# Optimization experiments

Hardware: AMD Instinct MI355X
Metric: run time of the kernel (lower is better)

## Reference

```python
import jax, jax.numpy as jnp
import numpy as np

B, L, C, H, FF = 4, 1024, 1024, 16, 4096
D = C // H  # head_dim = 64
SCALE = (D * 2.0) ** -0.5  # scale_factor = 2.0


def layer_norm(x, g, b, eps=1e-5):
    mu = jnp.mean(x, axis=-1, keepdims=True)
    var = jnp.var(x, axis=-1, keepdims=True)
    return (x - mu) * jax.lax.rsqrt(var + eps) * g + b


def setup_inputs() -> dict:
    key = jax.random.key(0)
    ks = jax.random.split(key, 12)
    s = 0.02
    inp = {
        'x': jax.random.normal(ks[0], (B, L, C), jnp.float32),
        'attn_bias': jax.random.normal(ks[1], (B, H, L, L), jnp.float32),
        'attention_mask': jnp.zeros((B, 1, L, L), jnp.float32),
        'Wq': jax.random.normal(ks[2], (C, C), jnp.float32) * s,
        'bq': jnp.zeros((C,), jnp.float32),
        'Wk': jax.random.normal(ks[3], (C, C), jnp.float32) * s,
        'bk': jnp.zeros((C,), jnp.float32),
        'Wv': jax.random.normal(ks[4], (C, C), jnp.float32) * s,
        'bv': jnp.zeros((C,), jnp.float32),
        'Wo': jax.random.normal(ks[5], (C, C), jnp.float32) * s,
        'bo': jnp.zeros((C,), jnp.float32),
        'c_attn': jnp.ones((H,), jnp.float32),
        'W1': jax.random.normal(ks[6], (FF, C), jnp.float32) * s,
        'b1': jnp.zeros((FF,), jnp.float32),
        'W2': jax.random.normal(ks[7], (C, FF), jnp.float32) * s,
        'b2': jnp.zeros((C,), jnp.float32),
        'attn_ln_g': jnp.ones((C,), jnp.float32),
        'attn_ln_b': jnp.zeros((C,), jnp.float32),
        'attn_mid_ln_g': jnp.ones((C,), jnp.float32),
        'attn_mid_ln_b': jnp.zeros((C,), jnp.float32),
        'ffn_ln_g': jnp.ones((C,), jnp.float32),
        'ffn_ln_b': jnp.zeros((C,), jnp.float32),
        'ffn_mid_ln_g': jnp.ones((FF,), jnp.float32),
        'ffn_mid_ln_b': jnp.zeros((FF,), jnp.float32),
    }
    return inp


def reference(x, attn_bias, attention_mask, Wq, bq, Wk, bk, Wv, bv, Wo, bo,
              c_attn, W1, b1, W2, b2, attn_ln_g, attn_ln_b,
              attn_mid_ln_g, attn_mid_ln_b, ffn_ln_g, ffn_ln_b,
              ffn_mid_ln_g, ffn_mid_ln_b):
    # ---- attention block (pre-norm, normformer) ----
    residual = x
    h = layer_norm(x, attn_ln_g, attn_ln_b)
    q = (h @ Wq.T + bq).reshape(B, L, H, D).transpose(0, 2, 1, 3)  # (B,H,L,D)
    k = (h @ Wk.T + bk).reshape(B, L, H, D).transpose(0, 2, 1, 3)
    v = (h @ Wv.T + bv).reshape(B, L, H, D).transpose(0, 2, 1, 3)
    # scores with bias (src_len == tgt_len, so the -src_len: slice is full) and mask
    scores = jnp.einsum('bhld,bhsd->bhls', q, k) * SCALE + attn_bias + attention_mask
    w = jax.nn.softmax(scores, axis=-1)
    attn = jnp.einsum('bhls,bhsd->bhld', w, v)
    attn = attn * c_attn[None, :, None, None]  # per-head scale (scale_heads)
    attn = attn.transpose(0, 2, 1, 3).reshape(B, L, C)
    attn = attn @ Wo.T + bo
    attn = layer_norm(attn, attn_mid_ln_g, attn_mid_ln_b)  # normformer mid-LN
    x = residual + attn
    # ---- FFN block (pre-norm, normformer) ----
    residual = x
    h = layer_norm(x, ffn_ln_g, ffn_ln_b)
    h = jax.nn.gelu(h @ W1.T + b1, approximate=False)
    h = layer_norm(h, ffn_mid_ln_g, ffn_mid_ln_b)  # normformer mid-LN on d_ff
    h = h @ W2.T + b2
    x = residual + h
    return x
```

## Files before the change

### kernel.cpp

```cpp
#include <hip/hip_runtime.h>
#include <hip/hip_bf16.h>
#include <math.h>

#define BB 4
#define LL 1024
#define CC 1024
#define HH 16
#define DD 64
#define FFD 4096
#define MM (BB*LL)
#define ATT_SCALE 0.08838834764831845f

typedef __bf16 bf16x8 __attribute__((ext_vector_type(8)));
typedef float f32x4 __attribute__((ext_vector_type(4)));

#define F32_PATTERN 0x3F800000u

__device__ __forceinline__ float b2f(unsigned short u) {
  union { unsigned int i; float f; } v; v.i = ((unsigned int)u) << 16; return v.f;
}
__device__ __forceinline__ unsigned short f2b(float f) {
  union { float f; unsigned int i; } v; v.f = f;
  unsigned int x = v.i;
  return (unsigned short)((x + 0x7fffu + ((x >> 16) & 1u)) >> 16);
}
__device__ __forceinline__ float ld1(const void* p, size_t i, bool isf32) {
  return isf32 ? reinterpret_cast<const float*>(p)[i]
               : b2f(reinterpret_cast<const unsigned short*>(p)[i]);
}
__device__ __forceinline__ float4 ld4(const void* p, size_t i, bool isf32) {
  float4 r;
  if (isf32) {
    r = *reinterpret_cast<const float4*>(reinterpret_cast<const float*>(p) + i);
  } else {
    ushort4 u = *reinterpret_cast<const ushort4*>(reinterpret_cast<const unsigned short*>(p) + i);
    r.x = b2f(u.x); r.y = b2f(u.y); r.z = b2f(u.z); r.w = b2f(u.w);
  }
  return r;
}
__device__ __forceinline__ float wave_sum(float v) {
#pragma unroll
  for (int o = 32; o > 0; o >>= 1) v += __shfl_down(v, o, 64);
  return v;
}

typedef __attribute__((address_space(1))) const void* as1cv;
typedef __attribute__((address_space(3))) void* as3v;
__device__ __forceinline__ void glds16(const void* g, void* l) {
  __builtin_amdgcn_global_load_lds((as1cv)g, (as3v)l, 16, 0, 0);
}

template <int COLS>
__global__ __launch_bounds__(256) void k_ln(
    const void* __restrict__ src, int srcext,
    const void* __restrict__ g, const void* __restrict__ bta,
    const void* __restrict__ res,
    unsigned short* __restrict__ dst,
    const unsigned int* __restrict__ probe)
{
  const bool isf32 = (*probe == F32_PATTERN);
  const bool sf = srcext && isf32;
  constexpr int NCH = COLS / 1024;
  const int row = blockIdx.x;
  const int t = threadIdx.x;
  const size_t base = (size_t)row * COLS;
  float fv[NCH * 4];
  float s = 0.f, s2 = 0.f;
#pragma unroll
  for (int c = 0; c < NCH; ++c) {
    float4 u = ld4(src, base + (size_t)(t + 256 * c) * 4, sf);
    fv[c * 4 + 0] = u.x; fv[c * 4 + 1] = u.y; fv[c * 4 + 2] = u.z; fv[c * 4 + 3] = u.w;
    s += u.x + u.y + u.z + u.w;
    s2 += u.x * u.x + u.y * u.y + u.z * u.z + u.w * u.w;
  }
  s = wave_sum(s); s2 = wave_sum(s2);
  __shared__ float red1[4], red2[4], stats[2];
  const int wv = t >> 6;
  if ((t & 63) == 0) { red1[wv] = s; red2[wv] = s2; }
  __syncthreads();
  if (t == 0) {
    float S = red1[0] + red1[1] + red1[2] + red1[3];
    float S2 = red2[0] + red2[1] + red2[2] + red2[3];
    float mu = S / COLS;
    float var = S2 / COLS - mu * mu;
    stats[0] = mu; stats[1] = rsqrtf(fmaxf(var, 0.f) + 1e-5f);
  }
  __syncthreads();
  const float mu = stats[0], rsg = stats[1];
#pragma unroll
  for (int c = 0; c < NCH; ++c) {
    const int off = (t + 256 * c) * 4;
    float4 gv = ld4(g, off, isf32);
    float4 bv = ld4(bta, off, isf32);
    float r0 = 0.f, r1 = 0.f, r2 = 0.f, r3 = 0.f;
    if (res) {
      float4 rv = ld4(res, base + off, isf32);
      r0 = rv.x; r1 = rv.y; r2 = rv.z; r3 = rv.w;
    }
    ushort4 o;
    o.x = f2b((fv[c * 4 + 0] - mu) * rsg * gv.x + bv.x + r0);
    o.y = f2b((fv[c * 4 + 1] - mu) * rsg * gv.y + bv.y + r1);
    o.z = f2b((fv[c * 4 + 2] - mu) * rsg * gv.z + bv.z + r2);
    o.w = f2b((fv[c * 4 + 3] - mu) * rsg * gv.w + bv.w + r3);
    *reinterpret_cast<ushort4*>(&dst[base + off]) = o;
  }
}

__global__ __launch_bounds__(256) void k_w2b(
    const void* __restrict__ Wq, const void* __restrict__ Wk,
    const void* __restrict__ Wv, const void* __restrict__ Wo,
    const void* __restrict__ W1, const void* __restrict__ W2,
    unsigned short* __restrict__ dst, const unsigned int* __restrict__ probe)
{
  const bool isf32 = (*probe == F32_PATTERN);
  const size_t NW = (size_t)CC * CC;
  const size_t i = ((size_t)blockIdx.x * 256 + threadIdx.x) * 8;
  const void* src; size_t off;
  if      (i <     NW) { src = Wq; off = i; }
  else if (i < 2 * NW) { src = Wk; off = i - NW; }
  else if (i < 3 * NW) { src = Wv; off = i - 2 * NW; }
  else if (i < 4 * NW) { src = Wo; off = i - 3 * NW; }
  else if (i < 8 * NW) { src = W1; off = i - 4 * NW; }
  else                 { src = W2; off = i - 8 * NW; }
  ushort4 lo, hi;
  if (isf32) {
    const float* f = reinterpret_cast<const float*>(src) + off;
    float4 u = *reinterpret_cast<const float4*>(f);
    float4 v = *reinterpret_cast<const float4*>(f + 4);
    lo.x = f2b(u.x); lo.y = f2b(u.y); lo.z = f2b(u.z); lo.w = f2b(u.w);
    hi.x = f2b(v.x); hi.y = f2b(v.y); hi.z = f2b(v.z); hi.w = f2b(v.w);
  } else {
    const unsigned short* u = reinterpret_cast<const unsigned short*>(src) + off;
    lo = *reinterpret_cast<const ushort4*>(u);
    hi = *reinterpret_cast<const ushort4*>(u + 4);
  }
  *reinterpret_cast<ushort4*>(&dst[i])     = lo;
  *reinterpret_cast<ushort4*>(&dst[i + 4]) = hi;
}

template <int EPI, int NT>
__device__ __forceinline__ void gemm_core(
    const unsigned short* __restrict__ A,
    const unsigned short* __restrict__ W,
    const void* __restrict__ bias,
    const unsigned short* __restrict__ res,
    void* __restrict__ out, int outext,
    int M, int N, int K, bool isf32)
{
  constexpr int BN = NT * 32;
  __shared__ __align__(16) unsigned short As[128][32];
  __shared__ __align__(16) unsigned short Bs[BN][32];
  const int t = threadIdx.x;
  const int wv = t >> 6, lane = t & 63;
  const int fr = lane & 15, kq = (lane >> 4) * 8;
  const int gx = gridDim.x;
  const int nwg = gx * gridDim.y;
  int lin = blockIdx.y * gx + blockIdx.x;
  if ((nwg & 7) == 0) lin = (lin & 7) * (nwg >> 3) + (lin >> 3);
  const int m0 = (lin / gx) * 128, n0 = (lin % gx) * BN;
  const int wr = (wv >> 1) * 64, wc = (wv & 1) * (BN / 2);

  f32x4 acc[4][NT];
#pragma unroll
  for (int i = 0; i < 4; ++i)
#pragma unroll
    for (int j = 0; j < NT; ++j) acc[i][j] = (f32x4){0.f, 0.f, 0.f, 0.f};

  const int sr = t >> 2, sc = (t & 3) * 8;
  const unsigned short* ga = &A[(size_t)(m0 + sr) * K + sc];
  const unsigned short* gb = &W[(size_t)(n0 + sr) * K + sc];
  unsigned short* la = &As[0][0] + t * 8;
  unsigned short* lb = &Bs[0][0] + t * 8;
  const size_t rstep = (size_t)64 * K;

  for (int k0 = 0; k0 < K; k0 += 32) {
    __syncthreads();
    glds16(ga + k0, la);
    glds16(ga + rstep + k0, la + 2048);
    glds16(gb + k0, lb);
    if (NT == 4) glds16(gb + rstep + k0, lb + 2048);
    __syncthreads();
    bf16x8 af[4], wf[NT];
#pragma unroll
    for (int mi = 0; mi < 4; ++mi)
      af[mi] = *reinterpret_cast<const bf16x8*>(&As[wr + mi * 16 + fr][kq]);
#pragma unroll
    for (int ni = 0; ni < NT; ++ni)
      wf[ni] = *reinterpret_cast<const bf16x8*>(&Bs[wc + ni * 16 + fr][kq]);
#pragma unroll
    for (int mi = 0; mi < 4; ++mi)
#pragma unroll
      for (int ni = 0; ni < NT; ++ni)
        acc[mi][ni] = __builtin_amdgcn_mfma_f32_16x16x32_bf16(af[mi], wf[ni], acc[mi][ni], 0, 0, 0);
  }

  const int q4 = (lane >> 4) * 4;
#pragma unroll
  for (int ni = 0; ni < NT; ++ni) {
    const int n = n0 + wc + ni * 16 + fr;
    const float bv = ld1(bias, n, isf32);
#pragma unroll
    for (int mi = 0; mi < 4; ++mi) {
#pragma unroll
      for (int r = 0; r < 4; ++r) {
        const int m = m0 + wr + mi * 16 + q4 + r;
        float vv = acc[mi][ni][r] + bv;
        if (EPI == 1) vv = 0.5f * vv * (1.f + erff(vv * 0.70710678118654752f));
        if (EPI == 2) vv += b2f(res[(size_t)m * N + n]);
        const size_t oi = (size_t)m * N + n;
        if (outext && isf32) reinterpret_cast<float*>(out)[oi] = vv;
        else                 reinterpret_cast<unsigned short*>(out)[oi] = f2b(vv);
      }
    }
  }
}

template <int EPI, int NT>
__global__ __launch_bounds__(256) void k_gemm(
    const unsigned short* __restrict__ A,
    const unsigned short* __restrict__ W,
    const void* __restrict__ bias,
    const unsigned short* __restrict__ res,
    void* __restrict__ out, int outext,
    int M, int N, int K,
    const unsigned int* __restrict__ probe)
{
  const bool isf32 = (*probe == F32_PATTERN);
  gemm_core<EPI, NT>(A, W, bias, res, out, outext, M, N, K, isf32);
}

__global__ __launch_bounds__(256) void k_gemm_qkv(
    const unsigned short* __restrict__ A,
    const unsigned short* __restrict__ Wqb, const unsigned short* __restrict__ Wkb,
    const unsigned short* __restrict__ Wvb,
    const void* __restrict__ bq, const void* __restrict__ bk, const void* __restrict__ bv,
    unsigned short* __restrict__ oq, unsigned short* __restrict__ ok,
    unsigned short* __restrict__ ov,
    const unsigned int* __restrict__ probe)
{
  const bool isf32 = (*probe == F32_PATTERN);
  const int z = blockIdx.z;
  const unsigned short* W = (z == 0) ? Wqb : (z == 1) ? Wkb : Wvb;
  const void* bias = (z == 0) ? bq : (z == 1) ? bk : bv;
  unsigned short* out = (z == 0) ? oq : (z == 1) ? ok : ov;
  gemm_core<0, 4>(A, W, bias, nullptr, out, 0, MM, CC, CC, isf32);
}

__global__ __launch_bounds__(512) void k_attn(
    const unsigned short* __restrict__ Q,
    const unsigned short* __restrict__ K,
    const unsigned short* __restrict__ V,
    const void* __restrict__ bias,
    const void* __restrict__ mask,
    const void* __restrict__ c_attn,
    unsigned short* __restrict__ ctx,
    const unsigned int* __restrict__ probe)
{
  const bool isf32 = (*probe == F32_PATTERN);
  const int qt = blockIdx.x, h = blockIdx.y, b = blockIdx.z;
  const int q0 = qt * 128;
  const int t = threadIdx.x;
  const int wv = t >> 6, lane = t & 63;
  const int a = lane & 15, quad = lane >> 4;

  __shared__ __align__(16) unsigned short Qs[128][72];
  __shared__ __align__(16) unsigned short Ks[64][72];
  __shared__ __align__(16) unsigned short Ps[128][72];
  __shared__ __align__(16) unsigned short Vt[64 * 66];

  {
    const int r = t >> 2, c0 = (t & 3) * 16;
    const unsigned short* qp = &Q[((size_t)(b * LL + q0 + r)) * CC + h * DD + c0];
    *reinterpret_cast<int4*>(&Qs[r][c0])     = *reinterpret_cast<const int4*>(qp);
    *reinterpret_cast<int4*>(&Qs[r][c0 + 8]) = *reinterpret_cast<const int4*>(qp + 8);
  }

  f32x4 Sacc[4], Oacc[4];
  float m_old[4] = {-1e30f, -1e30f, -1e30f, -1e30f};
  float l_run[4] = {0.f, 0.f, 0.f, 0.f};
#pragma unroll
  for (int i = 0; i < 4; ++i) Oacc[i] = (f32x4){0.f, 0.f, 0.f, 0.f};

  const int vd = t & 63, vs0 = (t >> 6) * 8;
  const int kr = t >> 3, kc0 = (t & 7) * 8;
  const int qrow_lane = wv * 16 + quad * 4;
  const size_t bias_row0 = ((size_t)(b * HH + h) * LL + q0) * LL;
  const size_t mask_row0 = ((size_t)(b * LL + q0)) * LL;

  for (int scn = 0; scn < 16; ++scn) {
    const int s0 = scn * 64;
    const unsigned short* kp = &K[((size_t)(b * LL + s0 + kr)) * CC + h * DD + kc0];
    const int4 kv0 = *reinterpret_cast<const int4*>(kp);
    const unsigned short* vp = &V[((size_t)(b * LL + s0 + vs0)) * CC + h * DD + vd];
    unsigned short vvb[8];
#pragma unroll
    for (int j = 0; j < 8; ++j) vvb[j] = vp[(size_t)j * CC];
    float bm[16];
#pragma unroll
    for (int r = 0; r < 4; ++r) {
      const size_t br = bias_row0 + (size_t)(qrow_lane + r) * LL + s0 + a;
      const size_t mr = mask_row0 + (size_t)(qrow_lane + r) * LL + s0 + a;
#pragma unroll
      for (int nt = 0; nt < 4; ++nt)
        bm[r * 4 + nt] = ld1(bias, br + nt * 16, isf32) + ld1(mask, mr + nt * 16, isf32);
    }
    __syncthreads();
    *reinterpret_cast<int4*>(&Ks[kr][kc0]) = kv0;
#pragma unroll
    for (int j = 0; j < 4; ++j) {
      ushort2 p; p.x = vvb[2 * j]; p.y = vvb[2 * j + 1];
      *reinterpret_cast<ushort2*>(&Vt[vd * 66 + vs0 + 2 * j]) = p;
    }
    __syncthreads();
#pragma unroll
    for (int nt = 0; nt < 4; ++nt) Sacc[nt] = (f32x4){0.f, 0.f, 0.f, 0.f};
#pragma unroll
    for (int ks = 0; ks < 2; ++ks) {
      bf16x8 af = *reinterpret_cast<const bf16x8*>(&Qs[wv * 16 + a][ks * 32 + quad * 8]);
#pragma unroll
      for (int nt = 0; nt < 4; ++nt) {
        bf16x8 bf = *reinterpret_cast<const bf16x8*>(&Ks[nt * 16 + a][ks * 32 + quad * 8]);
        Sacc[nt] = __builtin_amdgcn_mfma_f32_16x16x32_bf16(af, bf, Sacc[nt], 0, 0, 0);
      }
    }
#pragma unroll
    for (int r = 0; r < 4; ++r)
#pragma unroll
      for (int nt = 0; nt < 4; ++nt)
        Sacc[nt][r] = Sacc[nt][r] * ATT_SCALE + bm[r * 4 + nt];
#pragma unroll
    for (int r = 0; r < 4; ++r) {
      float mc = fmaxf(fmaxf(Sacc[0][r], Sacc[1][r]), fmaxf(Sacc[2][r], Sacc[3][r]));
      mc = fmaxf(mc, __shfl_xor(mc, 1, 64));
      mc = fmaxf(mc, __shfl_xor(mc, 2, 64));
      mc = fmaxf(mc, __shfl_xor(mc, 4, 64));
      mc = fmaxf(mc, __shfl_xor(mc, 8, 64));
      const float mn = fmaxf(m_old[r], mc);
      const float al = __expf(m_old[r] - mn);
      m_old[r] = mn;
      float ps = 0.f;
#pragma unroll
      for (int nt = 0; nt < 4; ++nt) {
        const float p = __expf(Sacc[nt][r] - mn);
        Sacc[nt][r] = p;
        ps += p;
      }
      ps += __shfl_xor(ps, 1, 64);
      ps += __shfl_xor(ps, 2, 64);
      ps += __shfl_xor(ps, 4, 64);
      ps += __shfl_xor(ps, 8, 64);
      l_run[r] = l_run[r] * al + ps;
#pragma unroll
      for (int dt = 0; dt < 4; ++dt) Oacc[dt][r] *= al;
    }
#pragma unroll
    for (int r = 0; r < 4; ++r)
#pragma unroll
      for (int nt = 0; nt < 4; ++nt)
        Ps[qrow_lane + r][nt * 16 + a] = f2b(Sacc[nt][r]);
    __syncthreads();
#pragma unroll
    for (int ks = 0; ks < 2; ++ks) {
      bf16x8 pf = *reinterpret_cast<const bf16x8*>(&Ps[wv * 16 + a][ks * 32 + quad * 8]);
#pragma unroll
      for (int dt = 0; dt < 4; ++dt) {
        union { ushort2 u2[4]; bf16x8 v; } u;
        const unsigned short* vp2 = &Vt[(dt * 16 + a) * 66 + ks * 32 + quad * 8];
        u.u2[0] = *reinterpret_cast<const ushort2*>(vp2);
        u.u2[1] = *reinterpret_cast<const ushort2*>(vp2 + 2);
        u.u2[2] = *reinterpret_cast<const ushort2*>(vp2 + 4);
        u.u2[3] = *reinterpret_cast<const ushort2*>(vp2 + 6);
        Oacc[dt] = __builtin_amdgcn_mfma_f32_16x16x32_bf16(pf, u.v, Oacc[dt], 0, 0, 0);
      }
    }
  }
  const float cah = ld1(c_attn, h, isf32);
#pragma unroll
  for (int r = 0; r < 4; ++r) {
    const float inv = cah / fmaxf(l_run[r], 1e-30f);
    unsigned short* op = &ctx[((size_t)(b * LL + q0 + qrow_lane + r)) * CC + h * DD + a];
#pragma unroll
    for (int dt = 0; dt < 4; ++dt)
      op[dt * 16] = f2b(Oacc[dt][r] * inv);
  }
}

extern "C" void kernel_launch(void* const* d_in, const int* in_sizes, int n_in,
                              void* d_out, int out_size, void* d_ws, size_t ws_size,
                              hipStream_t stream) {
  (void)in_sizes; (void)n_in; (void)out_size; (void)ws_size;
  const void* x    = d_in[0];
  const void* abia = d_in[1];
  const void* amsk = d_in[2];
  const void* Wq   = d_in[3];
  const void* bq   = d_in[4];
  const void* Wk   = d_in[5];
  const void* bk   = d_in[6];
  const void* Wv   = d_in[7];
  const void* bv   = d_in[8];
  const void* Wo   = d_in[9];
  const void* bo   = d_in[10];
  const void* ca   = d_in[11];
  const void* W1   = d_in[12];
  const void* b1   = d_in[13];
  const void* W2   = d_in[14];
  const void* b2   = d_in[15];
  const void* alg  = d_in[16];
  const void* alb  = d_in[17];
  const void* amg  = d_in[18];
  const void* amb  = d_in[19];
  const void* flg  = d_in[20];
  const void* flb  = d_in[21];
  const void* fmg  = d_in[22];
  const void* fmb  = d_in[23];
  const unsigned int* probe = (const unsigned int*)alg;

  unsigned short* S0 = (unsigned short*)d_ws;
  unsigned short* S1 = S0 + (size_t)MM * CC;
  unsigned short* S2 = S1 + (size_t)MM * CC;
  unsigned short* S3 = S2 + (size_t)MM * CC;
  unsigned short* S4 = S3 + (size_t)MM * CC;
  unsigned short* S5 = S4 + (size_t)MM * CC;
  unsigned short* WB = S5 + (size_t)MM * CC;
  unsigned short* Wqb = WB;
  unsigned short* Wkb = WB + (size_t)CC * CC;
  unsigned short* Wvb = WB + (size_t)2 * CC * CC;
  unsigned short* Wob = WB + (size_t)3 * CC * CC;
  unsigned short* W1b = WB + (size_t)4 * CC * CC;
  unsigned short* W2b = W1b + (size_t)FFD * CC;

  dim3 blk(256);
  dim3 blkA(512);
  dim3 g1n(CC / 64, MM / 128);
  dim3 g2(FFD / 128, MM / 128);
  dim3 gqkv(CC / 128, MM / 128, 3);
  dim3 ga(LL / 128, HH, BB);

  k_w2b<<<6144, blk, 0, stream>>>(Wq, Wk, Wv, Wo, W1, W2, WB, probe);
  k_ln<CC><<<MM, blk, 0, stream>>>(x, 1, alg, alb, nullptr, S0, probe);
  k_gemm_qkv<<<gqkv, blk, 0, stream>>>(S0, Wqb, Wkb, Wvb, bq, bk, bv, S1, S2, S3, probe);
  k_attn<<<ga, blkA, 0, stream>>>(S1, S2, S3, abia, amsk, ca, S4, probe);
  k_gemm<0, 2><<<g1n, blk, 0, stream>>>(S4, Wob, bo, nullptr, S5, 0, MM, CC, CC, probe);
  k_ln<CC><<<MM, blk, 0, stream>>>(S5, 0, amg, amb, x, S1, probe);
  k_ln<CC><<<MM, blk, 0, stream>>>(S1, 0, flg, flb, nullptr, S0, probe);
  k_gemm<1, 4><<<g2, blk, 0, stream>>>(S0, W1b, b1, nullptr, S2, 0, MM, FFD, CC, probe);
  k_ln<FFD><<<MM, blk, 0, stream>>>(S2, 0, fmg, fmb, nullptr, S2, probe);
  k_gemm<2, 2><<<g1n, blk, 0, stream>>>(S2, W2b, b2, S1, d_out, 1, MM, CC, FFD, probe);
}
```

Measured before the change: 789.5 us.

## Double-buffer LDS tiles in GEMM and attention to overlap loads with MFMA

The GEMM core now uses two LDS buffers for the A and W tiles. It prefetches the next K-slice with global_load_lds while MFMAs run on the current slice, and uses one waitcnt+barrier per iteration instead of two __syncthreads. The attention kernel gets ping-pong K/V LDS buffers and register prefetch of the next chunk's K, V and bias/mask, so global latency is hidden behind the QK/PV compute. This costs more LDS and registers per block, which may reduce occupancy.

```diff
diff --git a/kernel.cpp b/kernel.cpp
--- a/kernel.cpp
+++ b/kernel.cpp
@@ -48,6 +48,13 @@
 typedef __attribute__((address_space(3))) void* as3v;
 __device__ __forceinline__ void glds16(const void* g, void* l) {
   __builtin_amdgcn_global_load_lds((as1cv)g, (as3v)l, 16, 0, 0);
+}
+
+__device__ __forceinline__ void bar_vm0() {
+  asm volatile("s_waitcnt vmcnt(0)\n\ts_barrier" ::: "memory");
+}
+__device__ __forceinline__ void bar_lgkm() {
+  asm volatile("s_waitcnt lgkmcnt(0)\n\ts_barrier" ::: "memory");
 }
 
 template <int COLS>
@@ -148,8 +155,10 @@
     int M, int N, int K, bool isf32)
 {
   constexpr int BN = NT * 32;
-  __shared__ __align__(16) unsigned short As[128][32];
-  __shared__ __align__(16) unsigned short Bs[BN][32];
+  constexpr int ABUF = 128 * 32;
+  constexpr int BBUF = BN * 32;
+  __shared__ __align__(16) unsigned short As[2][128][32];
+  __shared__ __align__(16) unsigned short Bs[2][BN][32];
   const int t = threadIdx.x;
   const int wv = t >> 6, lane = t & 63;
   const int fr = lane & 15, kq = (lane >> 4) * 8;
@@ -169,29 +178,41 @@
   const int sr = t >> 2, sc = (t & 3) * 8;
   const unsigned short* ga = &A[(size_t)(m0 + sr) * K + sc];
   const unsigned short* gb = &W[(size_t)(n0 + sr) * K + sc];
-  unsigned short* la = &As[0][0] + t * 8;
-  unsigned short* lb = &Bs[0][0] + t * 8;
+  unsigned short* la = &As[0][0][0] + t * 8;
+  unsigned short* lb = &Bs[0][0][0] + t * 8;
   const size_t rstep = (size_t)64 * K;
 
+  glds16(ga, la);
+  glds16(ga + rstep, la + 2048);
+  glds16(gb, lb);
+  if (NT == 4) glds16(gb + rstep, lb + 2048);
+  bar_vm0();
+
   for (int k0 = 0; k0 < K; k0 += 32) {
-    __syncthreads();
-    glds16(ga + k0, la);
-    glds16(ga + rstep + k0, la + 2048);
-    glds16(gb + k0, lb);
-    if (NT == 4) glds16(gb + rstep + k0, lb + 2048);
-    __syncthreads();
+    const int cur = (k0 >> 5) & 1;
+    if (k0 + 32 < K) {
+      const unsigned short* ga2 = ga + k0 + 32;
+      const unsigned short* gb2 = gb + k0 + 32;
+      unsigned short* la2 = la + (cur ^ 1) * ABUF;
+      unsigned short* lb2 = lb + (cur ^ 1) * BBUF;
+      glds16(ga2, la2);
+      glds16(ga2 + rstep, la2 + 2048);
+      glds16(gb2, lb2);
+      if (NT == 4) glds16(gb2 + rstep, lb2 + 2048);
+    }
     bf16x8 af[4], wf[NT];
 #pragma unroll
     for (int mi = 0; mi < 4; ++mi)
-      af[mi] = *reinterpret_cast<const bf16x8*>(&As[wr + mi * 16 + fr][kq]);
+      af[mi] = *reinterpret_cast<const bf16x8*>(&As[cur][wr + mi * 16 + fr][kq]);
 #pragma unroll
     for (int ni = 0; ni < NT; ++ni)
-      wf[ni] = *reinterpret_cast<const bf16x8*>(&Bs[wc + ni * 16 + fr][kq]);
+      wf[ni] = *reinterpret_cast<const bf16x8*>(&Bs[cur][wc + ni * 16 + fr][kq]);
 #pragma unroll
     for (int mi = 0; mi < 4; ++mi)
 #pragma unroll
       for (int ni = 0; ni < NT; ++ni)
         acc[mi][ni] = __builtin_amdgcn_mfma_f32_16x16x32_bf16(af[mi], wf[ni], acc[mi][ni], 0, 0, 0);
+    bar_vm0();
   }
 
   const int q4 = (lane >> 4) * 4;
@@ -264,22 +285,9 @@
   const int a = lane & 15, quad = lane >> 4;
 
   __shared__ __align__(16) unsigned short Qs[128][72];
-  __shared__ __align__(16) unsigned short Ks[64][72];
   __shared__ __align__(16) unsigned short Ps[128][72];
-  __shared__ __align__(16) unsigned short Vt[64 * 66];
-
-  {
-    const int r = t >> 2, c0 = (t & 3) * 16;
-    const unsigned short* qp = &Q[((size_t)(b * LL + q0 + r)) * CC + h * DD + c0];
-    *reinterpret_cast<int4*>(&Qs[r][c0])     = *reinterpret_cast<const int4*>(qp);
-    *reinterpret_cast<int4*>(&Qs[r][c0 + 8]) = *reinterpret_cast<const int4*>(qp + 8);
-  }
-
-  f32x4 Sacc[4], Oacc[4];
-  float m_old[4] = {-1e30f, -1e30f, -1e30f, -1e30f};
-  float l_run[4] = {0.f, 0.f, 0.f, 0.f};
-#pragma unroll
-  for (int i = 0; i < 4; ++i) Oacc[i] = (f32x4){0.f, 0.f, 0.f, 0.f};
+  __shared__ __align__(16) unsigned short Ks[2][64][72];
+  __shared__ __align__(16) unsigned short Vt[2][64 * 66];
 
   const int vd = t & 63, vs0 = (t >> 6) * 8;
   const int kr = t >> 3, kc0 = (t & 7) * 8;
@@ -287,31 +295,62 @@
   const size_t bias_row0 = ((size_t)(b * HH + h) * LL + q0) * LL;
   const size_t mask_row0 = ((size_t)(b * LL + q0)) * LL;
 
-  for (int scn = 0; scn < 16; ++scn) {
-    const int s0 = scn * 64;
-    const unsigned short* kp = &K[((size_t)(b * LL + s0 + kr)) * CC + h * DD + kc0];
+  f32x4 Sacc[4], Oacc[4];
+  float m_old[4] = {-1e30f, -1e30f, -1e30f, -1e30f};
+  float l_run[4] = {0.f, 0.f, 0.f, 0.f};
+#pragma unroll
+  for (int i = 0; i < 4; ++i) Oacc[i] = (f32x4){0.f, 0.f, 0.f, 0.f};
+
+  float bm[16];
+  {
+    const unsigned short* kp = &K[((size_t)(b * LL + kr)) * CC + h * DD + kc0];
     const int4 kv0 = *reinterpret_cast<const int4*>(kp);
-    const unsigned short* vp = &V[((size_t)(b * LL + s0 + vs0)) * CC + h * DD + vd];
+    const unsigned short* vp = &V[((size_t)(b * LL + vs0)) * CC + h * DD + vd];
     unsigned short vvb[8];
 #pragma unroll
     for (int j = 0; j < 8; ++j) vvb[j] = vp[(size_t)j * CC];
-    float bm[16];
 #pragma unroll
     for (int r = 0; r < 4; ++r) {
-      const size_t br = bias_row0 + (size_t)(qrow_lane + r) * LL + s0 + a;
-      const size_t mr = mask_row0 + (size_t)(qrow_lane + r) * LL + s0 + a;
+      const size_t br = bias_row0 + (size_t)(qrow_lane + r) * LL + a;
+      const size_t mr = mask_row0 + (size_t)(qrow_lane + r) * LL + a;
 #pragma unroll
       for (int nt = 0; nt < 4; ++nt)
         bm[r * 4 + nt] = ld1(bias, br + nt * 16, isf32) + ld1(mask, mr + nt * 16, isf32);
     }
-    __syncthreads();
-    *reinterpret_cast<int4*>(&Ks[kr][kc0]) = kv0;
+    const int r = t >> 2, c0 = (t & 3) * 16;
+    const unsigned short* qp = &Q[((size_t)(b * LL + q0 + r)) * CC + h * DD + c0];
+    *reinterpret_cast<int4*>(&Qs[r][c0])     = *reinterpret_cast<const int4*>(qp);
+    *reinterpret_cast<int4*>(&Qs[r][c0 + 8]) = *reinterpret_cast<const int4*>(qp + 8);
+    *reinterpret_cast<int4*>(&Ks[0][kr][kc0]) = kv0;
 #pragma unroll
     for (int j = 0; j < 4; ++j) {
       ushort2 p; p.x = vvb[2 * j]; p.y = vvb[2 * j + 1];
-      *reinterpret_cast<ushort2*>(&Vt[vd * 66 + vs0 + 2 * j]) = p;
-    }
-    __syncthreads();
+      *reinterpret_cast<ushort2*>(&Vt[0][vd * 66 + vs0 + 2 * j]) = p;
+    }
+  }
+  bar_lgkm();
+
+  for (int scn = 0; scn < 16; ++scn) {
+    const int x = scn & 1;
+    int4 kvn;
+    unsigned short vvbn[8];
+    float bmn[16];
+    if (scn < 15) {
+      const int s0n = (scn + 1) * 64;
+      const unsigned short* kp = &K[((size_t)(b * LL + s0n + kr)) * CC + h * DD + kc0];
+      kvn = *reinterpret_cast<const int4*>(kp);
+      const unsigned short* vp = &V[((size_t)(b * LL + s0n + vs0)) * CC + h * DD + vd];
+#pragma unroll
+      for (int j = 0; j < 8; ++j) vvbn[j] = vp[(size_t)j * CC];
+#pragma unroll
+      for (int r = 0; r < 4; ++r) {
+        const size_t br = bias_row0 + (size_t)(qrow_lane + r) * LL + s0n + a;
+        const size_t mr = mask_row0 + (size_t)(qrow_lane + r) * LL + s0n + a;
+#pragma unroll
+        for (int nt = 0; nt < 4; ++nt)
+          bmn[r * 4 + nt] = ld1(bias, br + nt * 16, isf32) + ld1(mask, mr + nt * 16, isf32);
+      }
+    }
 #pragma unroll
     for (int nt = 0; nt < 4; ++nt) Sacc[nt] = (f32x4){0.f, 0.f, 0.f, 0.f};
 #pragma unroll
@@ -319,7 +358,7 @@
       bf16x8 af = *reinterpret_cast<const bf16x8*>(&Qs[wv * 16 + a][ks * 32 + quad * 8]);
 #pragma unroll
       for (int nt = 0; nt < 4; ++nt) {
-        bf16x8 bf = *reinterpret_cast<const bf16x8*>(&Ks[nt * 16 + a][ks * 32 + quad * 8]);
+        bf16x8 bf = *reinterpret_cast<const bf16x8*>(&Ks[x][nt * 16 + a][ks * 32 + quad * 8]);
         Sacc[nt] = __builtin_amdgcn_mfma_f32_16x16x32_bf16(af, bf, Sacc[nt], 0, 0, 0);
       }
     }
@@ -358,20 +397,33 @@
 #pragma unroll
       for (int nt = 0; nt < 4; ++nt)
         Ps[qrow_lane + r][nt * 16 + a] = f2b(Sacc[nt][r]);
-    __syncthreads();
+    bar_lgkm();
 #pragma unroll
     for (int ks = 0; ks < 2; ++ks) {
       bf16x8 pf = *reinterpret_cast<const bf16x8*>(&Ps[wv * 16 + a][ks * 32 + quad * 8]);
 #pragma unroll
       for (int dt = 0; dt < 4; ++dt) {
         union { ushort2 u2[4]; bf16x8 v; } u;
-        const unsigned short* vp2 = &Vt[(dt * 16 + a) * 66 + ks * 32 + quad * 8];
+        const unsigned short* vp2 = &Vt[x][(dt * 16 + a) * 66 + ks * 32 + quad * 8];
         u.u2[0] = *reinterpret_cast<const ushort2*>(vp2);
         u.u2[1] = *reinterpret_cast<const ushort2*>(vp2 + 2);
         u.u2[2] = *reinterpret_cast<const ushort2*>(vp2 + 4);
         u.u2[3] = *reinterpret_cast<const ushort2*>(vp2 + 6);
         Oacc[dt] = __builtin_amdgcn_mfma_f32_16x16x32_bf16(pf, u.v, Oacc[dt], 0, 0, 0);
       }
+    }
+    if (scn < 15) {
+      *reinterpret_cast<int4*>(&Ks[x ^ 1][kr][kc0]) = kvn;
+#pragma unroll
+      for (int j = 0; j < 4; ++j) {
+        ushort2 p; p.x = vvbn[2 * j]; p.y = vvbn[2 * j + 1];
+        *reinterpret_cast<ushort2*>(&Vt[x ^ 1][vd * 66 + vs0 + 2 * j]) = p;
+      }
+    }
+    bar_lgkm();
+    if (scn < 15) {
+#pragma unroll
+      for (int i = 0; i < 16; ++i) bm[i] = bmn[i];
     }
   }
   const float cah = ld1(c_attn, h, isf32);
```

After: 759.2 us. -3.8%, faster.
